# Kernel tuning notes

Measured on AMD Instinct MI355X. Metric: run time of the kernel, lower is better.

The kernel has to match this reference:

```python
import jax, jax.numpy as jnp
import numpy as np
import math

B, NH, SQ, HD = 4, 32, 512, 128
MLEN = 3584


def setup_inputs() -> dict:
    key = jax.random.key(0)
    k1, k2, k3, k4 = jax.random.split(key, 4)
    q = jax.random.normal(k1, (B, NH, SQ, HD), dtype=jnp.float32)
    k = jax.random.normal(k2, (B, NH, SQ, HD), dtype=jnp.float32)
    v = jax.random.normal(k3, (B, NH, SQ, HD), dtype=jnp.float32)
    mem = jax.random.normal(k4, (B, MLEN, 2 * NH * HD), dtype=jnp.float32)
    mask = jnp.ones((B, 1, SQ, MLEN + SQ), dtype=jnp.float32)
    return {"q": q, "k": k, "v": v, "mask": mask, "mem": mem}


def reference(q, k, v, mask, mem):
    b, nh, sq, hd = k.shape
    mlen = mem.shape[1]
    # cache_kv: stack (k,v) -> (2,b,nh,sq,hd), permute -> (b,sq,2,nh,hd), flatten
    cache_kv = jnp.stack((k, v)).transpose(1, 3, 0, 2, 4).reshape(b, sq, 2 * nh * hd)
    # split cached mem into memk/memv: (b,mlen,2,nh,hd) -> (2,b,nh,mlen,hd)
    mem_r = mem.reshape(b, mlen, 2, nh, hd).transpose(2, 0, 3, 1, 4)
    k_full = jnp.concatenate([mem_r[0], k], axis=2)  # [b,nh,mlen+sq,hd]
    v_full = jnp.concatenate([mem_r[1], v], axis=2)
    scale = 1.0 / math.sqrt(hd)
    scores = jnp.einsum("bhqd,bhkd->bhqk", q * scale, k_full)
    # standard_attention general mask path (mask.shape[-2] != 1)
    scores = scores * mask - 10000.0 * (1.0 - mask)
    probs = jax.nn.softmax(scores, axis=-1)
    context = jnp.einsum("bhqk,bhkd->bhqd", probs, v_full)
    return context, cache_kv
```

## Files before the change

### kernel.cpp

```cpp
#include <hip/hip_runtime.h>

#define B_ 4
#define NH_ 32
#define SQ_ 512
#define HD_ 128
#define MLEN_ 3584
#define KT_ 4096
#define QB_ 128
#define KB_ 64
#define NTILE_ 64
#define MEMTILES_ 56

typedef float f32x4 __attribute__((ext_vector_type(4)));
typedef short s16x8 __attribute__((ext_vector_type(8)));

__device__ __forceinline__ f32x4 MFMA16(s16x8 a, s16x8 b, f32x4 c) {
    return __builtin_amdgcn_mfma_f32_16x16x32_bf16(a, b, c, 0, 0, 0);
}

__device__ __forceinline__ s16x8 cvt8(float4 a, float4 b) {
    union { s16x8 v; __bf16 h[8]; } u;
    u.h[0] = (__bf16)a.x; u.h[1] = (__bf16)a.y;
    u.h[2] = (__bf16)a.z; u.h[3] = (__bf16)a.w;
    u.h[4] = (__bf16)b.x; u.h[5] = (__bf16)b.y;
    u.h[6] = (__bf16)b.z; u.h[7] = (__bf16)b.w;
    return u.v;
}

__launch_bounds__(512, 4)
__global__ void attn_kernel(const float* __restrict__ q, const float* __restrict__ k,
                            const float* __restrict__ v, const float* __restrict__ mask,
                            const float* __restrict__ mem, float* __restrict__ ctx)
{
    __shared__ __bf16 Klds[KB_ * HD_];
    __shared__ __bf16 Vt[HD_ * KB_];

    const int tid  = threadIdx.x;
    const int lane = tid & 63;
    const int w    = tid >> 6;
    const int l15  = lane & 15;
    const int l4   = lane >> 4;
    const int xv   = (lane & 7) << 4;

    const int qt   = blockIdx.x >> 7;
    const int pair = blockIdx.x & 127;
    const int b    = pair >> 5;
    const int h    = pair & 31;
    const int q0   = qt * QB_;

    const float scale = 0.088388347648318447f;
    s16x8 qf[4];
    {
        const float* qbase = q + (((size_t)(b * NH_ + h)) * SQ_ + q0 + w * 16 + l15) * HD_;
        #pragma unroll
        for (int kc = 0; kc < 4; ++kc) {
            const float* p = qbase + kc * 32 + l4 * 8;
            float4 a = *(const float4*)p;
            float4 c = *(const float4*)(p + 4);
            a.x *= scale; a.y *= scale; a.z *= scale; a.w *= scale;
            c.x *= scale; c.y *= scale; c.z *= scale; c.w *= scale;
            qf[kc] = cvt8(a, c);
        }
    }

    f32x4 acc[8];
    #pragma unroll
    for (int n = 0; n < 8; ++n) acc[n] = (f32x4){0.f, 0.f, 0.f, 0.f};

    float mrun = -3.0e38f, lrun = 0.f;

    const float* maskrow = mask + ((size_t)b * SQ_ + q0 + w * 16 + l15) * KT_;

    for (int t = 0; t < NTILE_; ++t) {
        const int kv0 = t * KB_;
        const float *srcK, *srcV;
        int rstride;
        if (t < MEMTILES_) {
            const float* mrow = mem + ((size_t)b * MLEN_ + kv0) * (2 * NH_ * HD_) + h * HD_;
            srcK = mrow;
            srcV = mrow + NH_ * HD_;
            rstride = 2 * NH_ * HD_;
        } else {
            size_t off = (((size_t)b * NH_ + h) * SQ_ + (kv0 - MLEN_)) * HD_;
            srcK = k + off;
            srcV = v + off;
            rstride = HD_;
        }

        __syncthreads();

        #pragma unroll
        for (int it = 0; it < 2; ++it) {
            int idx = tid + it * 512;
            int row = idx >> 4, cg = idx & 15;
            const float* p = srcK + (size_t)row * rstride + cg * 8;
            float4 a = *(const float4*)p;
            float4 c = *(const float4*)(p + 4);
            s16x8 vv = cvt8(a, c);
            int byte = row * 256 + ((cg * 16) ^ ((row & 7) << 4));
            *(s16x8*)((char*)Klds + byte) = vv;
        }
        #pragma unroll
        for (int it = 0; it < 2; ++it) {
            int idx = tid + it * 512;
            int hd = idx & 127, kvb = idx >> 7;
            const float* p = srcV + (size_t)(kvb * 8) * rstride + hd;
            union { s16x8 v; __bf16 hh[8]; } u;
            #pragma unroll
            for (int j = 0; j < 8; ++j) u.hh[j] = (__bf16)p[(size_t)j * rstride];
            int byte = hd * 128 + ((kvb * 16) ^ ((hd & 7) << 4));
            *(s16x8*)((char*)Vt + byte) = u.v;
        }

        __syncthreads();

        f32x4 mk[4];
        #pragma unroll
        for (int mt = 0; mt < 4; ++mt)
            mk[mt] = *(const f32x4*)(maskrow + kv0 + mt * 16 + l4 * 4);

        f32x4 st[4];
        #pragma unroll
        for (int mt = 0; mt < 4; ++mt) st[mt] = (f32x4){0.f, 0.f, 0.f, 0.f};
        #pragma unroll
        for (int mt = 0; mt < 4; ++mt) {
            #pragma unroll
            for (int kc = 0; kc < 4; ++kc) {
                s16x8 kf = *(const s16x8*)((const char*)Klds +
                            (mt * 16 + l15) * 256 + (((kc * 4 + l4) * 16) ^ xv));
                st[mt] = MFMA16(kf, qf[kc], st[mt]);
            }
        }

        #pragma unroll
        for (int mt = 0; mt < 4; ++mt)
            #pragma unroll
            for (int r = 0; r < 4; ++r)
                st[mt][r] = fmaf(mk[mt][r], st[mt][r] + 10000.f, -10000.f);

        float x0 = fmaxf(fmaxf(st[0][0], st[0][1]), fmaxf(st[0][2], st[0][3]));
        float x1 = fmaxf(fmaxf(st[1][0], st[1][1]), fmaxf(st[1][2], st[1][3]));
        float x2 = fmaxf(fmaxf(st[2][0], st[2][1]), fmaxf(st[2][2], st[2][3]));
        float x3 = fmaxf(fmaxf(st[3][0], st[3][1]), fmaxf(st[3][2], st[3][3]));
        float rm = fmaxf(fmaxf(x0, x1), fmaxf(x2, x3));
        rm = fmaxf(rm, __shfl_xor(rm, 16));
        rm = fmaxf(rm, __shfl_xor(rm, 32));

        if (!__all(rm <= mrun + 8.f)) {
            float nm = fmaxf(mrun, rm);
            float al = __expf(mrun - nm);
            mrun = nm;
            lrun *= al;
            float alr0 = __shfl(al, l4 * 4 + 0);
            float alr1 = __shfl(al, l4 * 4 + 1);
            float alr2 = __shfl(al, l4 * 4 + 2);
            float alr3 = __shfl(al, l4 * 4 + 3);
            #pragma unroll
            for (int nn = 0; nn < 8; ++nn) {
                acc[nn][0] *= alr0; acc[nn][1] *= alr1;
                acc[nn][2] *= alr2; acc[nn][3] *= alr3;
            }
        }

        float rs = 0.f;
        #pragma unroll
        for (int mt = 0; mt < 4; ++mt) {
            #pragma unroll
            for (int r = 0; r < 4; ++r) {
                float pe = __expf(st[mt][r] - mrun);
                st[mt][r] = pe;
                rs += pe;
            }
        }
        rs += __shfl_xor(rs, 16);
        rs += __shfl_xor(rs, 32);
        lrun += rs;

        union PK { int d[2]; __bf16 hh[4]; };
        PK pk0, pk1, pk2, pk3;
        pk0.hh[0]=(__bf16)st[0][0]; pk0.hh[1]=(__bf16)st[0][1]; pk0.hh[2]=(__bf16)st[0][2]; pk0.hh[3]=(__bf16)st[0][3];
        pk1.hh[0]=(__bf16)st[1][0]; pk1.hh[1]=(__bf16)st[1][1]; pk1.hh[2]=(__bf16)st[1][2]; pk1.hh[3]=(__bf16)st[1][3];
        pk2.hh[0]=(__bf16)st[2][0]; pk2.hh[1]=(__bf16)st[2][1]; pk2.hh[2]=(__bf16)st[2][2]; pk2.hh[3]=(__bf16)st[2][3];
        pk3.hh[0]=(__bf16)st[3][0]; pk3.hh[1]=(__bf16)st[3][1]; pk3.hh[2]=(__bf16)st[3][2]; pk3.hh[3]=(__bf16)st[3][3];

        const int srcA = (l4 & 1) * 32 + l15;
        const int srcB = srcA + 16;
        const int sel  = l4 >> 1;
        s16x8 pa[2];
        {
            union { int d[4]; s16x8 v; } ua;
            int a00 = __shfl(pk0.d[0], srcA), a10 = __shfl(pk1.d[0], srcA);
            int a01 = __shfl(pk0.d[1], srcA), a11 = __shfl(pk1.d[1], srcA);
            int b00 = __shfl(pk0.d[0], srcB), b10 = __shfl(pk1.d[0], srcB);
            int b01 = __shfl(pk0.d[1], srcB), b11 = __shfl(pk1.d[1], srcB);
            ua.d[0] = sel ? a10 : a00; ua.d[1] = sel ? a11 : a01;
            ua.d[2] = sel ? b10 : b00; ua.d[3] = sel ? b11 : b01;
            pa[0] = ua.v;
        }
        {
            union { int d[4]; s16x8 v; } ua;
            int a00 = __shfl(pk2.d[0], srcA), a10 = __shfl(pk3.d[0], srcA);
            int a01 = __shfl(pk2.d[1], srcA), a11 = __shfl(pk3.d[1], srcA);
            int b00 = __shfl(pk2.d[0], srcB), b10 = __shfl(pk3.d[0], srcB);
            int b01 = __shfl(pk2.d[1], srcB), b11 = __shfl(pk3.d[1], srcB);
            ua.d[0] = sel ? a10 : a00; ua.d[1] = sel ? a11 : a01;
            ua.d[2] = sel ? b10 : b00; ua.d[3] = sel ? b11 : b01;
            pa[1] = ua.v;
        }

        #pragma unroll
        for (int nn = 0; nn < 8; ++nn) {
            s16x8 vf0 = *(const s16x8*)((const char*)Vt +
                          (nn * 16 + l15) * 128 + ((l4 * 16) ^ xv));
            s16x8 vf1 = *(const s16x8*)((const char*)Vt +
                          (nn * 16 + l15) * 128 + ((64 + l4 * 16) ^ xv));
            acc[nn] = MFMA16(pa[0], vf0, acc[nn]);
            acc[nn] = MFMA16(pa[1], vf1, acc[nn]);
        }
    }

    float lr0 = __shfl(lrun, l4 * 4 + 0);
    float lr1 = __shfl(lrun, l4 * 4 + 1);
    float lr2 = __shfl(lrun, l4 * 4 + 2);
    float lr3 = __shfl(lrun, l4 * 4 + 3);
    float inv0 = 1.f / lr0, inv1 = 1.f / lr1, inv2 = 1.f / lr2, inv3 = 1.f / lr3;
    float* obase = ctx + (((size_t)(b * NH_ + h)) * SQ_ + q0 + w * 16 + l4 * 4) * HD_ + l15;
    #pragma unroll
    for (int nn = 0; nn < 8; ++nn) {
        obase[(size_t)0 * HD_ + nn * 16] = acc[nn][0] * inv0;
        obase[(size_t)1 * HD_ + nn * 16] = acc[nn][1] * inv1;
        obase[(size_t)2 * HD_ + nn * 16] = acc[nn][2] * inv2;
        obase[(size_t)3 * HD_ + nn * 16] = acc[nn][3] * inv3;
    }
}

__global__ void cachekv_kernel(const float* __restrict__ k, const float* __restrict__ v,
                               float* __restrict__ out)
{
    size_t i = ((size_t)blockIdx.x * 256 + threadIdx.x) * 4;
    unsigned f = (unsigned)i;
    unsigned d    = f & 127;
    unsigned hh   = (f >> 7) & 31;
    unsigned part = (f >> 12) & 1;
    unsigned s    = (f >> 13) & 511;
    unsigned bb   = f >> 22;
    const float* src = (part ? v : k) + (((size_t)(bb * 32u + hh)) * 512u + s) * 128u + d;
    *(float4*)(out + i) = *(const float4*)src;
}

extern "C" void kernel_launch(void* const* d_in, const int* in_sizes, int n_in,
                              void* d_out, int out_size, void* d_ws, size_t ws_size,
                              hipStream_t stream) {
    const float* q    = (const float*)d_in[0];
    const float* k    = (const float*)d_in[1];
    const float* v    = (const float*)d_in[2];
    const float* mask = (const float*)d_in[3];
    const float* mem  = (const float*)d_in[4];
    float* out = (float*)d_out;

    attn_kernel<<<dim3(B_ * NH_ * (SQ_ / QB_)), dim3(512), 0, stream>>>(q, k, v, mask, mem, out);

    const int ctx_elems = B_ * NH_ * SQ_ * HD_;
    const int ckv_elems = B_ * SQ_ * 2 * NH_ * HD_;
    cachekv_kernel<<<dim3(ckv_elems / 4 / 256), dim3(256), 0, stream>>>(k, v, out + ctx_elems);
    (void)in_sizes; (void)n_in; (void)out_size; (void)d_ws; (void)ws_size;
}
```

Measured before the change: 322.1 us.

## Double-buffer K/V tiles in LDS with register prefetch two tiles ahead

Splits the K/V staging into a global-load phase into registers and a later convert-and-store phase into one of two LDS buffers. Loads for tile t+2 are issued while tile t is computed, and tile t+1 is written to the other buffer. Each iteration now needs one barrier instead of two, and the mask is loaded ahead of use. In exchange LDS use and register pressure rise (prefetched floats held across the loop), which could lower occupancy under launch_bounds(512,4). The custom barrier only waits on lgkmcnt before s_barrier.

```diff
diff --git a/kernel.cpp b/kernel.cpp
--- a/kernel.cpp
+++ b/kernel.cpp
@@ -18,6 +18,10 @@
     return __builtin_amdgcn_mfma_f32_16x16x32_bf16(a, b, c, 0, 0, 0);
 }
 
+__device__ __forceinline__ void wg_barrier() {
+    asm volatile("s_waitcnt lgkmcnt(0)\n\ts_barrier" ::: "memory");
+}
+
 __device__ __forceinline__ s16x8 cvt8(float4 a, float4 b) {
     union { s16x8 v; __bf16 h[8]; } u;
     u.h[0] = (__bf16)a.x; u.h[1] = (__bf16)a.y;
@@ -32,8 +36,8 @@
                             const float* __restrict__ v, const float* __restrict__ mask,
                             const float* __restrict__ mem, float* __restrict__ ctx)
 {
-    __shared__ __bf16 Klds[KB_ * HD_];
-    __shared__ __bf16 Vt[HD_ * KB_];
+    __shared__ __bf16 Klds[2][KB_ * HD_];
+    __shared__ __bf16 Vt[2][HD_ * KB_];
 
     const int tid  = threadIdx.x;
     const int lane = tid & 63;
@@ -71,7 +75,14 @@
 
     const float* maskrow = mask + ((size_t)b * SQ_ + q0 + w * 16 + l15) * KT_;
 
-    for (int t = 0; t < NTILE_; ++t) {
+    const int krow = tid >> 4,  kcg  = tid & 15;
+    const int vhd  = tid & 127, vkvb = tid >> 7;
+
+    float4 kpa[2], kpb[2];
+    float  vpre[2][8];
+    f32x4  mk[4];
+
+    auto issueKV = [&](int t) {
         const int kv0 = t * KB_;
         const float *srcK, *srcV;
         int rstride;
@@ -86,38 +97,53 @@
             srcV = v + off;
             rstride = HD_;
         }
-
-        __syncthreads();
-
         #pragma unroll
         for (int it = 0; it < 2; ++it) {
-            int idx = tid + it * 512;
-            int row = idx >> 4, cg = idx & 15;
-            const float* p = srcK + (size_t)row * rstride + cg * 8;
-            float4 a = *(const float4*)p;
-            float4 c = *(const float4*)(p + 4);
-            s16x8 vv = cvt8(a, c);
-            int byte = row * 256 + ((cg * 16) ^ ((row & 7) << 4));
-            *(s16x8*)((char*)Klds + byte) = vv;
+            const float* p = srcK + (size_t)(krow + it * 32) * rstride + kcg * 8;
+            kpa[it] = *(const float4*)p;
+            kpb[it] = *(const float4*)(p + 4);
         }
         #pragma unroll
         for (int it = 0; it < 2; ++it) {
-            int idx = tid + it * 512;
-            int hd = idx & 127, kvb = idx >> 7;
-            const float* p = srcV + (size_t)(kvb * 8) * rstride + hd;
+            const float* p = srcV + (size_t)((vkvb + it * 4) * 8) * rstride + vhd;
+            #pragma unroll
+            for (int j = 0; j < 8; ++j) vpre[it][j] = p[(size_t)j * rstride];
+        }
+    };
+    auto writeKV = [&](int buf) {
+        #pragma unroll
+        for (int it = 0; it < 2; ++it) {
+            int row = krow + it * 32;
+            s16x8 vv = cvt8(float4{kpa[it].x, kpa[it].y, kpa[it].z, kpa[it].w},
+                            float4{kpb[it].x, kpb[it].y, kpb[it].z, kpb[it].w});
+            int byte = row * 256 + ((kcg * 16) ^ ((row & 7) << 4));
+            *(s16x8*)((char*)Klds[buf] + byte) = vv;
+        }
+        #pragma unroll
+        for (int it = 0; it < 2; ++it) {
+            int kvb = vkvb + it * 4;
             union { s16x8 v; __bf16 hh[8]; } u;
             #pragma unroll
-            for (int j = 0; j < 8; ++j) u.hh[j] = (__bf16)p[(size_t)j * rstride];
-            int byte = hd * 128 + ((kvb * 16) ^ ((hd & 7) << 4));
-            *(s16x8*)((char*)Vt + byte) = u.v;
-        }
-
-        __syncthreads();
-
-        f32x4 mk[4];
+            for (int j = 0; j < 8; ++j) u.hh[j] = (__bf16)vpre[it][j];
+            int byte = vhd * 128 + ((kvb * 16) ^ ((vhd & 7) << 4));
+            *(s16x8*)((char*)Vt[buf] + byte) = u.v;
+        }
+    };
+    auto loadmask = [&](int t) {
+        const int kv0 = t * KB_;
         #pragma unroll
         for (int mt = 0; mt < 4; ++mt)
             mk[mt] = *(const f32x4*)(maskrow + kv0 + mt * 16 + l4 * 4);
+    };
+
+    issueKV(0);
+    writeKV(0);
+    loadmask(0);
+    issueKV(1);
+    wg_barrier();
+
+    for (int t = 0; t < NTILE_; ++t) {
+        const int cur = t & 1;
 
         f32x4 st[4];
         #pragma unroll
@@ -126,7 +152,7 @@
         for (int mt = 0; mt < 4; ++mt) {
             #pragma unroll
             for (int kc = 0; kc < 4; ++kc) {
-                s16x8 kf = *(const s16x8*)((const char*)Klds +
+                s16x8 kf = *(const s16x8*)((const char*)Klds[cur] +
                             (mt * 16 + l15) * 256 + (((kc * 4 + l4) * 16) ^ xv));
                 st[mt] = MFMA16(kf, qf[kc], st[mt]);
             }
@@ -210,13 +236,20 @@
 
         #pragma unroll
         for (int nn = 0; nn < 8; ++nn) {
-            s16x8 vf0 = *(const s16x8*)((const char*)Vt +
+            s16x8 vf0 = *(const s16x8*)((const char*)Vt[cur] +
                           (nn * 16 + l15) * 128 + ((l4 * 16) ^ xv));
-            s16x8 vf1 = *(const s16x8*)((const char*)Vt +
+            s16x8 vf1 = *(const s16x8*)((const char*)Vt[cur] +
                           (nn * 16 + l15) * 128 + ((64 + l4 * 16) ^ xv));
             acc[nn] = MFMA16(pa[0], vf0, acc[nn]);
             acc[nn] = MFMA16(pa[1], vf1, acc[nn]);
         }
+
+        if (t + 1 < NTILE_) {
+            writeKV(cur ^ 1);
+            loadmask(t + 1);
+            if (t + 2 < NTILE_) issueKV(t + 2);
+        }
+        wg_barrier();
     }
 
     float lr0 = __shfl(lrun, l4 * 4 + 0);
```

Measured after the change: 528.4 us. +64.0%, slower.

## Double-buffer K/V tiles in LDS with register prefetch of next tile

Applied to the files above, without the earlier changes.

Adds ping-pong LDS buffers for K and V and issues the global loads for the next tile into registers before the QK^T and PV MFMA work of the current tile. The converted values are written to the other buffer after compute, so each iteration needs one barrier instead of two. The aim is to hide global load latency behind matrix math. In exchange LDS use doubles to 64KB per block and register pressure rises from the prefetched floats, which may reduce occupancy below the launch-bounds target of 4 blocks.

```diff
diff --git a/kernel.cpp b/kernel.cpp
--- a/kernel.cpp
+++ b/kernel.cpp
@@ -32,8 +32,8 @@
                             const float* __restrict__ v, const float* __restrict__ mask,
                             const float* __restrict__ mem, float* __restrict__ ctx)
 {
-    __shared__ __bf16 Klds[KB_ * HD_];
-    __shared__ __bf16 Vt[HD_ * KB_];
+    __shared__ __bf16 Klds[2][KB_ * HD_];
+    __shared__ __bf16 Vt[2][HD_ * KB_];
 
     const int tid  = threadIdx.x;
     const int lane = tid & 63;
@@ -71,53 +71,80 @@
 
     const float* maskrow = mask + ((size_t)b * SQ_ + q0 + w * 16 + l15) * KT_;
 
+    const int krow = tid >> 4,  kcg  = tid & 15;
+    const int vhd  = tid & 127, vkvb = tid >> 7;
+
+    {
+        const float* mrow = mem + ((size_t)b * MLEN_) * (2 * NH_ * HD_) + h * HD_;
+        const float* srcK = mrow;
+        const float* srcV = mrow + NH_ * HD_;
+        const int rstride = 2 * NH_ * HD_;
+        #pragma unroll
+        for (int it = 0; it < 2; ++it) {
+            int row = krow + it * 32;
+            const float* p = srcK + (size_t)row * rstride + kcg * 8;
+            float4 a = *(const float4*)p;
+            float4 c = *(const float4*)(p + 4);
+            int byte = row * 256 + ((kcg * 16) ^ ((row & 7) << 4));
+            *(s16x8*)((char*)Klds[0] + byte) = cvt8(a, c);
+        }
+        #pragma unroll
+        for (int it = 0; it < 2; ++it) {
+            int kvb = vkvb + it * 4;
+            const float* p = srcV + (size_t)(kvb * 8) * rstride + vhd;
+            union { s16x8 v; __bf16 hh[8]; } u;
+            #pragma unroll
+            for (int j = 0; j < 8; ++j) u.hh[j] = (__bf16)p[(size_t)j * rstride];
+            int byte = vhd * 128 + ((kvb * 16) ^ ((vhd & 7) << 4));
+            *(s16x8*)((char*)Vt[0] + byte) = u.v;
+        }
+    }
+    __syncthreads();
+
     for (int t = 0; t < NTILE_; ++t) {
+        const int cur = t & 1;
         const int kv0 = t * KB_;
+        const int tn  = (t + 1 < NTILE_) ? (t + 1) : (NTILE_ - 1);
+
+        f32x4 mk[4];
+        #pragma unroll
+        for (int mt = 0; mt < 4; ++mt)
+            mk[mt] = *(const f32x4*)(maskrow + kv0 + mt * 16 + l4 * 4);
+
         const float *srcK, *srcV;
         int rstride;
-        if (t < MEMTILES_) {
-            const float* mrow = mem + ((size_t)b * MLEN_ + kv0) * (2 * NH_ * HD_) + h * HD_;
-            srcK = mrow;
-            srcV = mrow + NH_ * HD_;
-            rstride = 2 * NH_ * HD_;
-        } else {
-            size_t off = (((size_t)b * NH_ + h) * SQ_ + (kv0 - MLEN_)) * HD_;
-            srcK = k + off;
-            srcV = v + off;
-            rstride = HD_;
-        }
-
-        __syncthreads();
-
-        #pragma unroll
-        for (int it = 0; it < 2; ++it) {
-            int idx = tid + it * 512;
-            int row = idx >> 4, cg = idx & 15;
-            const float* p = srcK + (size_t)row * rstride + cg * 8;
-            float4 a = *(const float4*)p;
-            float4 c = *(const float4*)(p + 4);
-            s16x8 vv = cvt8(a, c);
-            int byte = row * 256 + ((cg * 16) ^ ((row & 7) << 4));
-            *(s16x8*)((char*)Klds + byte) = vv;
-        }
-        #pragma unroll
-        for (int it = 0; it < 2; ++it) {
-            int idx = tid + it * 512;
-            int hd = idx & 127, kvb = idx >> 7;
-            const float* p = srcV + (size_t)(kvb * 8) * rstride + hd;
-            union { s16x8 v; __bf16 hh[8]; } u;
-            #pragma unroll
-            for (int j = 0; j < 8; ++j) u.hh[j] = (__bf16)p[(size_t)j * rstride];
-            int byte = hd * 128 + ((kvb * 16) ^ ((hd & 7) << 4));
-            *(s16x8*)((char*)Vt + byte) = u.v;
-        }
-
-        __syncthreads();
-
-        f32x4 mk[4];
-        #pragma unroll
-        for (int mt = 0; mt < 4; ++mt)
-            mk[mt] = *(const f32x4*)(maskrow + kv0 + mt * 16 + l4 * 4);
+        {
+            const int nkv0 = tn * KB_;
+            if (tn < MEMTILES_) {
+                const float* mrow = mem + ((size_t)b * MLEN_ + nkv0) * (2 * NH_ * HD_) + h * HD_;
+                srcK = mrow;
+                srcV = mrow + NH_ * HD_;
+                rstride = 2 * NH_ * HD_;
+            } else {
+                size_t off = (((size_t)b * NH_ + h) * SQ_ + (nkv0 - MLEN_)) * HD_;
+                srcK = k + off;
+                srcV = v + off;
+                rstride = HD_;
+            }
+        }
+        float4 ka0, kb0, ka1, kb1;
+        {
+            const float* p0 = srcK + (size_t)krow * rstride + kcg * 8;
+            ka0 = *(const float4*)p0;
+            kb0 = *(const float4*)(p0 + 4);
+            const float* p1 = srcK + (size_t)(krow + 32) * rstride + kcg * 8;
+            ka1 = *(const float4*)p1;
+            kb1 = *(const float4*)(p1 + 4);
+        }
+        float vp0[8], vp1[8];
+        {
+            const float* p0 = srcV + (size_t)(vkvb * 8) * rstride + vhd;
+            #pragma unroll
+            for (int j = 0; j < 8; ++j) vp0[j] = p0[(size_t)j * rstride];
+            const float* p1 = srcV + (size_t)((vkvb + 4) * 8) * rstride + vhd;
+            #pragma unroll
+            for (int j = 0; j < 8; ++j) vp1[j] = p1[(size_t)j * rstride];
+        }
 
         f32x4 st[4];
         #pragma unroll
@@ -126,7 +153,7 @@
         for (int mt = 0; mt < 4; ++mt) {
             #pragma unroll
             for (int kc = 0; kc < 4; ++kc) {
-                s16x8 kf = *(const s16x8*)((const char*)Klds +
+                s16x8 kf = *(const s16x8*)((const char*)Klds[cur] +
                             (mt * 16 + l15) * 256 + (((kc * 4 + l4) * 16) ^ xv));
                 st[mt] = MFMA16(kf, qf[kc], st[mt]);
             }
@@ -210,13 +237,34 @@
 
         #pragma unroll
         for (int nn = 0; nn < 8; ++nn) {
-            s16x8 vf0 = *(const s16x8*)((const char*)Vt +
+            s16x8 vf0 = *(const s16x8*)((const char*)Vt[cur] +
                           (nn * 16 + l15) * 128 + ((l4 * 16) ^ xv));
-            s16x8 vf1 = *(const s16x8*)((const char*)Vt +
+            s16x8 vf1 = *(const s16x8*)((const char*)Vt[cur] +
                           (nn * 16 + l15) * 128 + ((64 + l4 * 16) ^ xv));
             acc[nn] = MFMA16(pa[0], vf0, acc[nn]);
             acc[nn] = MFMA16(pa[1], vf1, acc[nn]);
         }
+
+        {
+            int row0 = krow;
+            int byte0 = row0 * 256 + ((kcg * 16) ^ ((row0 & 7) << 4));
+            *(s16x8*)((char*)Klds[cur ^ 1] + byte0) = cvt8(ka0, kb0);
+            int row1 = krow + 32;
+            int byte1 = row1 * 256 + ((kcg * 16) ^ ((row1 & 7) << 4));
+            *(s16x8*)((char*)Klds[cur ^ 1] + byte1) = cvt8(ka1, kb1);
+
+            union { s16x8 v; __bf16 hh[8]; } u0, u1;
+            #pragma unroll
+            for (int j = 0; j < 8; ++j) u0.hh[j] = (__bf16)vp0[j];
+            int vb0 = vhd * 128 + (((vkvb) * 16) ^ ((vhd & 7) << 4));
+            *(s16x8*)((char*)Vt[cur ^ 1] + vb0) = u0.v;
+            #pragma unroll
+            for (int j = 0; j < 8; ++j) u1.hh[j] = (__bf16)vp1[j];
+            int vb1 = vhd * 128 + (((vkvb + 4) * 16) ^ ((vhd & 7) << 4));
+            *(s16x8*)((char*)Vt[cur ^ 1] + vb1) = u1.v;
+        }
+
+        __syncthreads();
     }
 
     float lr0 = __shfl(lrun, l4 * 4 + 0);
```

Result: slower. 346.9 us (+7.7%).

## Prefetch K/V tiles into LDS asynchronously with double-buffered global_load_lds

Applied to the files above, without the earlier changes.

Each K/V tile is now brought into fp32 LDS buffers with async global_load_lds, two tiles ahead and double-buffered, and converted to bf16 from LDS rather than from registers. The KV tile shrinks from 64 to 32 rows so the fp32 staging fits, the LDS swizzles are redone, and the occupancy hint in launch_bounds is dropped. The goal is to hide the global-memory latency of the strided mem reads behind the MFMA and softmax work. The cost is more LDS, an extra LDS round trip for conversion, twice as many loop iterations with two barriers each, and possibly lower occupancy.

```diff
diff --git a/kernel.cpp b/kernel.cpp
--- a/kernel.cpp
+++ b/kernel.cpp
@@ -1,4 +1,5 @@
 #include <hip/hip_runtime.h>
+#include <stdint.h>
 
 #define B_ 4
 #define NH_ 32
@@ -7,15 +8,21 @@
 #define MLEN_ 3584
 #define KT_ 4096
 #define QB_ 128
-#define KB_ 64
-#define NTILE_ 64
-#define MEMTILES_ 56
+#define KB_ 32
+#define NTILE_ 128
+#define MEMTILES_ 112
 
 typedef float f32x4 __attribute__((ext_vector_type(4)));
 typedef short s16x8 __attribute__((ext_vector_type(8)));
 
 __device__ __forceinline__ f32x4 MFMA16(s16x8 a, s16x8 b, f32x4 c) {
     return __builtin_amdgcn_mfma_f32_16x16x32_bf16(a, b, c, 0, 0, 0);
+}
+
+__device__ __forceinline__ void gload16(const float* g, void* l) {
+    __builtin_amdgcn_global_load_lds(
+        (const __attribute__((address_space(1))) void*)g,
+        (__attribute__((address_space(3))) void*)l, 16, 0, 0);
 }
 
 __device__ __forceinline__ s16x8 cvt8(float4 a, float4 b) {
@@ -27,20 +34,23 @@
     return u.v;
 }
 
-__launch_bounds__(512, 4)
+__launch_bounds__(512)
 __global__ void attn_kernel(const float* __restrict__ q, const float* __restrict__ k,
                             const float* __restrict__ v, const float* __restrict__ mask,
                             const float* __restrict__ mem, float* __restrict__ ctx)
 {
-    __shared__ __bf16 Klds[KB_ * HD_];
-    __shared__ __bf16 Vt[HD_ * KB_];
+    __shared__ float  F32K[2][KB_ * HD_];
+    __shared__ float  F32V[2][KB_ * HD_];
+    __shared__ __bf16 Kb[KB_ * HD_];
+    __shared__ __bf16 Vtb[HD_ * KB_];
 
     const int tid  = threadIdx.x;
     const int lane = tid & 63;
     const int w    = tid >> 6;
     const int l15  = lane & 15;
     const int l4   = lane >> 4;
-    const int xv   = (lane & 7) << 4;
+    const int r2   = lane >> 5;
+    const int c32  = lane & 31;
 
     const int qt   = blockIdx.x >> 7;
     const int pair = blockIdx.x & 127;
@@ -71,78 +81,80 @@
 
     const float* maskrow = mask + ((size_t)b * SQ_ + q0 + w * 16 + l15) * KT_;
 
+#define ISSUE_TILE(tt, p)                                                              \
+    {                                                                                  \
+        const int _kv0 = (tt) * KB_;                                                   \
+        const float *_sk, *_sv; int _rs;                                               \
+        if ((tt) < MEMTILES_) {                                                        \
+            const float* _m = mem + ((size_t)b * MLEN_ + _kv0) * (2 * NH_ * HD_) + h * HD_; \
+            _sk = _m; _sv = _m + NH_ * HD_; _rs = 2 * NH_ * HD_;                       \
+        } else {                                                                       \
+            size_t _o = (((size_t)b * NH_ + h) * SQ_ + (_kv0 - MLEN_)) * HD_;          \
+            _sk = k + _o; _sv = v + _o; _rs = HD_;                                     \
+        }                                                                              \
+        _Pragma("unroll")                                                              \
+        for (int _s = 0; _s < 2; ++_s) {                                               \
+            int _seg = w * 2 + _s;                                                     \
+            int _row = _seg * 2 + r2;                                                  \
+            gload16(_sk + (size_t)_row * _rs + c32 * 4, (char*)F32K[p] + _seg * 1024); \
+            gload16(_sv + (size_t)_row * _rs + c32 * 4, (char*)F32V[p] + _seg * 1024); \
+        }                                                                              \
+    }
+
+#define CVT_TILE(p)                                                                    \
+    {                                                                                  \
+        int _kr = tid >> 4, _kc = tid & 15;                                            \
+        const float* _s = &F32K[p][_kr * HD_ + _kc * 8];                               \
+        float4 _a = *(const float4*)_s;                                                \
+        float4 _c = *(const float4*)(_s + 4);                                          \
+        int _by = _kr * 256 + (((_kc ^ (_kr & 7)) & 15) << 4);                         \
+        *(s16x8*)((char*)Kb + _by) = cvt8(_a, _c);                                     \
+        int _hd = tid & 127, _kb = tid >> 7;                                           \
+        const float* _sv = &F32V[p][_kb * 8 * HD_ + _hd];                              \
+        union { s16x8 v; __bf16 hh[8]; } _u;                                           \
+        _Pragma("unroll")                                                              \
+        for (int _j = 0; _j < 8; ++_j) _u.hh[_j] = (__bf16)_sv[_j * HD_];              \
+        int _vb = _hd * 64 + (((_kb ^ _hd ^ (_hd >> 2)) & 3) << 4);                    \
+        *(s16x8*)((char*)Vtb + _vb) = _u.v;                                            \
+    }
+
+    ISSUE_TILE(0, 0);
+    ISSUE_TILE(1, 1);
+    __syncthreads();
+    CVT_TILE(0);
+    __syncthreads();
+
     for (int t = 0; t < NTILE_; ++t) {
+        const int p   = t & 1;
         const int kv0 = t * KB_;
-        const float *srcK, *srcV;
-        int rstride;
-        if (t < MEMTILES_) {
-            const float* mrow = mem + ((size_t)b * MLEN_ + kv0) * (2 * NH_ * HD_) + h * HD_;
-            srcK = mrow;
-            srcV = mrow + NH_ * HD_;
-            rstride = 2 * NH_ * HD_;
-        } else {
-            size_t off = (((size_t)b * NH_ + h) * SQ_ + (kv0 - MLEN_)) * HD_;
-            srcK = k + off;
-            srcV = v + off;
-            rstride = HD_;
-        }
-
-        __syncthreads();
-
-        #pragma unroll
-        for (int it = 0; it < 2; ++it) {
-            int idx = tid + it * 512;
-            int row = idx >> 4, cg = idx & 15;
-            const float* p = srcK + (size_t)row * rstride + cg * 8;
-            float4 a = *(const float4*)p;
-            float4 c = *(const float4*)(p + 4);
-            s16x8 vv = cvt8(a, c);
-            int byte = row * 256 + ((cg * 16) ^ ((row & 7) << 4));
-            *(s16x8*)((char*)Klds + byte) = vv;
-        }
-        #pragma unroll
-        for (int it = 0; it < 2; ++it) {
-            int idx = tid + it * 512;
-            int hd = idx & 127, kvb = idx >> 7;
-            const float* p = srcV + (size_t)(kvb * 8) * rstride + hd;
-            union { s16x8 v; __bf16 hh[8]; } u;
-            #pragma unroll
-            for (int j = 0; j < 8; ++j) u.hh[j] = (__bf16)p[(size_t)j * rstride];
-            int byte = hd * 128 + ((kvb * 16) ^ ((hd & 7) << 4));
-            *(s16x8*)((char*)Vt + byte) = u.v;
-        }
-
-        __syncthreads();
-
-        f32x4 mk[4];
-        #pragma unroll
-        for (int mt = 0; mt < 4; ++mt)
-            mk[mt] = *(const f32x4*)(maskrow + kv0 + mt * 16 + l4 * 4);
-
-        f32x4 st[4];
-        #pragma unroll
-        for (int mt = 0; mt < 4; ++mt) st[mt] = (f32x4){0.f, 0.f, 0.f, 0.f};
-        #pragma unroll
-        for (int mt = 0; mt < 4; ++mt) {
+
+        if (t + 2 < NTILE_) ISSUE_TILE(t + 2, p);
+
+        f32x4 mk0 = *(const f32x4*)(maskrow + kv0 + l4 * 4);
+        f32x4 mk1 = *(const f32x4*)(maskrow + kv0 + 16 + l4 * 4);
+
+        f32x4 st[2];
+        st[0] = (f32x4){0.f, 0.f, 0.f, 0.f};
+        st[1] = (f32x4){0.f, 0.f, 0.f, 0.f};
+        #pragma unroll
+        for (int mt = 0; mt < 2; ++mt) {
+            int kr = mt * 16 + l15;
             #pragma unroll
             for (int kc = 0; kc < 4; ++kc) {
-                s16x8 kf = *(const s16x8*)((const char*)Klds +
-                            (mt * 16 + l15) * 256 + (((kc * 4 + l4) * 16) ^ xv));
+                s16x8 kf = *(const s16x8*)((const char*)Kb +
+                            kr * 256 + ((((kc * 4 + l4) ^ (kr & 7)) & 15) << 4));
                 st[mt] = MFMA16(kf, qf[kc], st[mt]);
             }
         }
 
         #pragma unroll
-        for (int mt = 0; mt < 4; ++mt)
-            #pragma unroll
-            for (int r = 0; r < 4; ++r)
-                st[mt][r] = fmaf(mk[mt][r], st[mt][r] + 10000.f, -10000.f);
-
-        float x0 = fmaxf(fmaxf(st[0][0], st[0][1]), fmaxf(st[0][2], st[0][3]));
-        float x1 = fmaxf(fmaxf(st[1][0], st[1][1]), fmaxf(st[1][2], st[1][3]));
-        float x2 = fmaxf(fmaxf(st[2][0], st[2][1]), fmaxf(st[2][2], st[2][3]));
-        float x3 = fmaxf(fmaxf(st[3][0], st[3][1]), fmaxf(st[3][2], st[3][3]));
-        float rm = fmaxf(fmaxf(x0, x1), fmaxf(x2, x3));
+        for (int r = 0; r < 4; ++r) {
+            st[0][r] = fmaf(mk0[r], st[0][r] + 10000.f, -10000.f);
+            st[1][r] = fmaf(mk1[r], st[1][r] + 10000.f, -10000.f);
+        }
+
+        float rm = fmaxf(fmaxf(fmaxf(st[0][0], st[0][1]), fmaxf(st[0][2], st[0][3])),
+                         fmaxf(fmaxf(st[1][0], st[1][1]), fmaxf(st[1][2], st[1][3])));
         rm = fmaxf(rm, __shfl_xor(rm, 16));
         rm = fmaxf(rm, __shfl_xor(rm, 32));
 
@@ -164,59 +176,50 @@
 
         float rs = 0.f;
         #pragma unroll
-        for (int mt = 0; mt < 4; ++mt) {
+        for (int mt = 0; mt < 2; ++mt)
             #pragma unroll
             for (int r = 0; r < 4; ++r) {
                 float pe = __expf(st[mt][r] - mrun);
                 st[mt][r] = pe;
                 rs += pe;
             }
-        }
         rs += __shfl_xor(rs, 16);
         rs += __shfl_xor(rs, 32);
         lrun += rs;
 
         union PK { int d[2]; __bf16 hh[4]; };
-        PK pk0, pk1, pk2, pk3;
-        pk0.hh[0]=(__bf16)st[0][0]; pk0.hh[1]=(__bf16)st[0][1]; pk0.hh[2]=(__bf16)st[0][2]; pk0.hh[3]=(__bf16)st[0][3];
-        pk1.hh[0]=(__bf16)st[1][0]; pk1.hh[1]=(__bf16)st[1][1]; pk1.hh[2]=(__bf16)st[1][2]; pk1.hh[3]=(__bf16)st[1][3];
-        pk2.hh[0]=(__bf16)st[2][0]; pk2.hh[1]=(__bf16)st[2][1]; pk2.hh[2]=(__bf16)st[2][2]; pk2.hh[3]=(__bf16)st[2][3];
-        pk3.hh[0]=(__bf16)st[3][0]; pk3.hh[1]=(__bf16)st[3][1]; pk3.hh[2]=(__bf16)st[3][2]; pk3.hh[3]=(__bf16)st[3][3];
+        PK pk0, pk1;
+        pk0.hh[0]=(__bf16)st[0][0]; pk0.hh[1]=(__bf16)st[0][1];
+        pk0.hh[2]=(__bf16)st[0][2]; pk0.hh[3]=(__bf16)st[0][3];
+        pk1.hh[0]=(__bf16)st[1][0]; pk1.hh[1]=(__bf16)st[1][1];
+        pk1.hh[2]=(__bf16)st[1][2]; pk1.hh[3]=(__bf16)st[1][3];
 
         const int srcA = (l4 & 1) * 32 + l15;
         const int srcB = srcA + 16;
         const int sel  = l4 >> 1;
-        s16x8 pa[2];
+        s16x8 pa;
         {
             union { int d[4]; s16x8 v; } ua;
-            int a00 = __shfl(pk0.d[0], srcA), a10 = __shfl(pk1.d[0], srcA);
-            int a01 = __shfl(pk0.d[1], srcA), a11 = __shfl(pk1.d[1], srcA);
-            int b00 = __shfl(pk0.d[0], srcB), b10 = __shfl(pk1.d[0], srcB);
-            int b01 = __shfl(pk0.d[1], srcB), b11 = __shfl(pk1.d[1], srcB);
-            ua.d[0] = sel ? a10 : a00; ua.d[1] = sel ? a11 : a01;
-            ua.d[2] = sel ? b10 : b00; ua.d[3] = sel ? b11 : b01;
-            pa[0] = ua.v;
-        }
-        {
-            union { int d[4]; s16x8 v; } ua;
-            int a00 = __shfl(pk2.d[0], srcA), a10 = __shfl(pk3.d[0], srcA);
-            int a01 = __shfl(pk2.d[1], srcA), a11 = __shfl(pk3.d[1], srcA);
-            int b00 = __shfl(pk2.d[0], srcB), b10 = __shfl(pk3.d[0], srcB);
-            int b01 = __shfl(pk2.d[1], srcB), b11 = __shfl(pk3.d[1], srcB);
-            ua.d[0] = sel ? a10 : a00; ua.d[1] = sel ? a11 : a01;
-            ua.d[2] = sel ? b10 : b00; ua.d[3] = sel ? b11 : b01;
-            pa[1] = ua.v;
+            int a0 = __shfl(pk0.d[0], srcA), a1 = __shfl(pk0.d[1], srcA);
+            int b0 = __shfl(pk1.d[0], srcA), b1 = __shfl(pk1.d[1], srcA);
+            int a2 = __shfl(pk0.d[0], srcB), a3 = __shfl(pk0.d[1], srcB);
+            int b2 = __shfl(pk1.d[0], srcB), b3 = __shfl(pk1.d[1], srcB);
+            ua.d[0] = sel ? b0 : a0; ua.d[1] = sel ? b1 : a1;
+            ua.d[2] = sel ? b2 : a2; ua.d[3] = sel ? b3 : a3;
+            pa = ua.v;
         }
 
         #pragma unroll
         for (int nn = 0; nn < 8; ++nn) {
-            s16x8 vf0 = *(const s16x8*)((const char*)Vt +
-                          (nn * 16 + l15) * 128 + ((l4 * 16) ^ xv));
-            s16x8 vf1 = *(const s16x8*)((const char*)Vt +
-                          (nn * 16 + l15) * 128 + ((64 + l4 * 16) ^ xv));
-            acc[nn] = MFMA16(pa[0], vf0, acc[nn]);
-            acc[nn] = MFMA16(pa[1], vf1, acc[nn]);
-        }
+            int hdv = nn * 16 + l15;
+            s16x8 vf = *(const s16x8*)((const char*)Vtb +
+                         hdv * 64 + (((l4 ^ hdv ^ (hdv >> 2)) & 3) << 4));
+            acc[nn] = MFMA16(pa, vf, acc[nn]);
+        }
+
+        __syncthreads();
+        if (t + 1 < NTILE_) CVT_TILE((t + 1) & 1);
+        __syncthreads();
     }
 
     float lr0 = __shfl(lrun, l4 * 4 + 0);
```

New measurement: 430.4 us. +33.6%, slower.
